# Optimization experiments

Hardware: AMD Instinct MI355X
Metric: run time of the kernel (lower is better)

The kernel has to match this reference:

```python
import jax, jax.numpy as jnp
import numpy as np

B, S, D = 2, 4096, 256
H, DH, DM = 8, 32, 1024
ROPE_BASE = 10000.0
LN_EPS = 1e-5


def _layer_norm(x, g, b):
    mu = jnp.mean(x, axis=-1, keepdims=True)
    var = jnp.mean(jnp.square(x - mu), axis=-1, keepdims=True)
    return (x - mu) * jax.lax.rsqrt(var + LN_EPS) * g + b


def _rope(x):
    # x: [b, s, h, d_head]; lucidrains interleaved-pair RoPE
    s, d = x.shape[1], x.shape[-1]
    inv_freq = 1.0 / (ROPE_BASE ** (jnp.arange(0, d, 2, dtype=jnp.float32) / d))  # [d/2]
    freqs = jnp.arange(s, dtype=jnp.float32)[:, None] * inv_freq[None, :]          # [s, d/2]
    freqs = jnp.repeat(freqs, 2, axis=-1)                                          # [s, d]
    cos = jnp.cos(freqs)[None, :, None, :]
    sin = jnp.sin(freqs)[None, :, None, :]
    x1, x2 = x[..., 0::2], x[..., 1::2]
    rot = jnp.stack((-x2, x1), axis=-1).reshape(x.shape)
    return x * cos + rot * sin


def setup_inputs() -> dict:
    key = jax.random.key(0)
    ks = jax.random.split(key, 8)
    sw = 1.0 / np.sqrt(D)
    return {
        "x": jax.random.normal(ks[0], (B, S, D), jnp.float32),
        "Wq": jax.random.normal(ks[1], (D, D), jnp.float32) * sw,
        "Wk": jax.random.normal(ks[2], (D, D), jnp.float32) * sw,
        "Wv": jax.random.normal(ks[3], (D, D), jnp.float32) * sw,
        "Wo": jax.random.normal(ks[4], (D, D), jnp.float32) * sw,
        "ln1_g": jnp.ones((D,), jnp.float32),
        "ln1_b": jnp.zeros((D,), jnp.float32),
        "ln2_g": jnp.ones((D,), jnp.float32),
        "ln2_b": jnp.zeros((D,), jnp.float32),
        "W2": jax.random.normal(ks[5], (DM, D), jnp.float32) * sw,
        "b2": jnp.zeros((DM,), jnp.float32),
        "W3": jax.random.normal(ks[6], (D, DM), jnp.float32) * (1.0 / np.sqrt(DM)),
        "b3": jnp.zeros((D,), jnp.float32),
    }


def reference(x, Wq, Wk, Wv, Wo, ln1_g, ln1_b, ln2_g, ln2_b, W2, b2, W3, b3):
    b, s, d = x.shape
    h, dh = H, DH
    xn = _layer_norm(x, ln1_g, ln1_b)
    q = (xn @ Wq.T).reshape(b, s, h, dh)
    k = (xn @ Wk.T).reshape(b, s, h, dh)
    v = (xn @ Wv.T).reshape(b, s, h, dh)
    q = _rope(q)
    k = _rope(k)
    # scores: [b, h, q, k] (full matrix, matching original implementation)
    scores = jnp.einsum('bqhd,bkhd->bhqk', q, k) / np.sqrt(dh)
    attn = jax.nn.softmax(scores, axis=-1)
    out = jnp.einsum('bhqk,bkhd->bqhd', attn, v).reshape(b, s, d)
    out = out @ Wo.T
    mlp_in = out + x
    y = _layer_norm(mlp_in, ln2_g, ln2_b)
    y = jax.nn.gelu(y @ W2.T + b2, approximate=False)
    y = y @ W3.T + b3
    return y + mlp_in
```

## Files before the change

kernel.cpp:

```cpp
#include <hip/hip_runtime.h>
#include <math.h>

#define D 256
#define S 4096
#define H 8
#define DH 32
#define DM 1024
#define NTOK 8192

typedef __attribute__((ext_vector_type(8))) short short8;
typedef __attribute__((ext_vector_type(4))) float f32x4;

#define QSCALE (0.17677669529663687f * 1.4426950408889634f)

__device__ inline unsigned short f2bf(float f) {
    union { float f; unsigned u; } v; v.f = f;
    unsigned r = v.u + 0x7fffu + ((v.u >> 16) & 1u);
    return (unsigned short)(r >> 16);
}
__device__ inline void gload16(const void* g, void* l) {
    __builtin_amdgcn_global_load_lds((const __attribute__((address_space(1))) void*)g,
                                     (__attribute__((address_space(3))) void*)l, 16, 0, 0);
}

__global__ void conv_all(const float* __restrict__ Wq, const float* __restrict__ Wk,
                         const float* __restrict__ Wv, const float* __restrict__ Wo,
                         const float* __restrict__ W2, const float* __restrict__ W3,
                         unsigned short* __restrict__ wqkv, unsigned short* __restrict__ wo_b,
                         unsigned short* __restrict__ w2_b, unsigned short* __restrict__ w3_b,
                         float* __restrict__ ct, float* __restrict__ st) {
    int i = blockIdx.x * 256 + threadIdx.x;
    if (i < 196608) {
        const float* s = (i < 65536) ? Wq : ((i < 131072) ? Wk : Wv);
        wqkv[i] = f2bf(s[i & 65535]);
    } else if (i < 262144) {
        wo_b[i - 196608] = f2bf(Wo[i - 196608]);
    } else if (i < 524288) {
        w2_b[i - 262144] = f2bf(W2[i - 262144]);
    } else if (i < 786432) {
        w3_b[i - 524288] = f2bf(W3[i - 524288]);
    } else {
        int j = i - 786432;
        int spos = j >> 4, pi = j & 15;
        float inv_freq = powf(10000.0f, -(float)(2 * pi) / 32.0f);
        float fr = (float)spos * inv_freq;
        ct[j] = cosf(fr);
        st[j] = sinf(fr);
    }
}

__global__ void ln_kernel(const float* __restrict__ x, const float* __restrict__ g,
                          const float* __restrict__ b, unsigned short* __restrict__ out) {
    __shared__ float red[8];
    int row = blockIdx.x;
    int tid = threadIdx.x;
    float v = x[(size_t)row * D + tid];
    float s = v, s2 = v * v;
    #pragma unroll
    for (int off = 32; off > 0; off >>= 1) {
        s  += __shfl_xor(s, off, 64);
        s2 += __shfl_xor(s2, off, 64);
    }
    int wave = tid >> 6;
    if ((tid & 63) == 0) { red[wave] = s; red[wave + 4] = s2; }
    __syncthreads();
    float sum   = red[0] + red[1] + red[2] + red[3];
    float sumsq = red[4] + red[5] + red[6] + red[7];
    float mu  = sum * (1.0f / D);
    float var = sumsq * (1.0f / D) - mu * mu;
    float rs  = rsqrtf(var + 1e-5f);
    out[(size_t)row * D + tid] = f2bf((v - mu) * rs * g[tid] + b[tid]);
}

__global__ __launch_bounds__(256) void gemm128(const unsigned short* __restrict__ A,
        const unsigned short* __restrict__ Bw, void* __restrict__ outp,
        unsigned short* __restrict__ vt,
        const float* __restrict__ bias, const float* __restrict__ res,
        const float* __restrict__ ct, const float* __restrict__ st,
        int N, int K, int mode) {
    __shared__ unsigned short As[2][128 * 32];
    __shared__ unsigned short Bs[2][64 * 32];
    int tid = threadIdx.x;
    int w = tid >> 6, l = tid & 63;
    int lm = l & 15, lg = l >> 4;
    int wm = (w >> 1) * 64, wn = (w & 1) * 32;
    int bm = blockIdx.x * 128, bn = blockIdx.y * 64;
    const unsigned short* Ag = A + (size_t)(bm + w * 16 + (l >> 2)) * K + ((l & 3) ^ ((l >> 3) & 3)) * 8;
    const unsigned short* Bg = Bw + (size_t)(bn + w * 16 + (l >> 2)) * K + ((l & 3) ^ ((l >> 3) & 3)) * 8;
    const int kswz = (lm >> 1) & 3;
    f32x4 acc[4][2] = {};

    gload16(Ag, &As[0][w * 512]);
    gload16(Ag + (size_t)64 * K, &As[0][2048 + w * 512]);
    gload16(Bg, &Bs[0][w * 512]);
    #pragma unroll 2
    for (int k0 = 0; k0 < K; k0 += 32) {
        int cur = (k0 >> 5) & 1;
        __syncthreads();
        if (k0 + 32 < K) {
            gload16(Ag + k0 + 32, &As[1 - cur][w * 512]);
            gload16(Ag + (size_t)64 * K + k0 + 32, &As[1 - cur][2048 + w * 512]);
            gload16(Bg + k0 + 32, &Bs[1 - cur][w * 512]);
        }
        short8 af[4], bf[2];
        #pragma unroll
        for (int i = 0; i < 4; ++i) af[i] = *(const short8*)&As[cur][(wm + i * 16 + lm) * 32 + (lg ^ kswz) * 8];
        #pragma unroll
        for (int i = 0; i < 2; ++i) bf[i] = *(const short8*)&Bs[cur][(wn + i * 16 + lm) * 32 + (lg ^ kswz) * 8];
        #pragma unroll
        for (int mi = 0; mi < 4; ++mi)
            #pragma unroll
            for (int ni = 0; ni < 2; ++ni)
                acc[mi][ni] = __builtin_amdgcn_mfma_f32_16x16x32_bf16(af[mi], bf[ni], acc[mi][ni], 0, 0, 0);
    }

    if (mode == 0) {
        if (bn >= 512) {
            #pragma unroll
            for (int mi = 0; mi < 4; ++mi) {
                #pragma unroll
                for (int ni = 0; ni < 2; ++ni) {
                    int ng = bn + wn + ni * 16 + lm - 512;
                    int hh = ng >> 5, dh = ng & 31;
                    int mg0 = bm + wm + mi * 16 + lg * 4;
                    int bb = mg0 >> 12, ss = mg0 & 4095;
                    ushort4 pv;
                    pv.x = f2bf(acc[mi][ni][0]); pv.y = f2bf(acc[mi][ni][1]);
                    pv.z = f2bf(acc[mi][ni][2]); pv.w = f2bf(acc[mi][ni][3]);
                    *(ushort4*)(vt + ((size_t)((bb * 8 + hh) * 32 + dh)) * S + ss) = pv;
                }
            }
        } else {
            #pragma unroll
            for (int mi = 0; mi < 4; ++mi) {
                #pragma unroll
                for (int ni = 0; ni < 2; ++ni) {
                    int ng = bn + wn + ni * 16 + lm;
                    int pi = (ng & 31) >> 1;
                    float sgn = (ng & 1) ? 1.f : -1.f;
                    float qs  = (ng < 256) ? QSCALE : 1.f;
                    #pragma unroll
                    for (int r2 = 0; r2 < 4; ++r2) {
                        int mg = bm + wm + mi * 16 + lg * 4 + r2;
                        int spos = mg & (S - 1);
                        float vv = acc[mi][ni][r2];
                        float pv = __shfl_xor(vv, 1, 64);
                        float cs = ct[spos * 16 + pi];
                        float sn = st[spos * 16 + pi];
                        float ov = (vv * cs + sgn * pv * sn) * qs;
                        ((unsigned short*)outp)[(size_t)mg * N + ng] = f2bf(ov);
                    }
                }
            }
        }
        return;
    }
    #pragma unroll
    for (int mi = 0; mi < 4; ++mi) {
        #pragma unroll
        for (int ni = 0; ni < 2; ++ni) {
            int ng = bn + wn + ni * 16 + lm;
            #pragma unroll
            for (int r2 = 0; r2 < 4; ++r2) {
                int mg = bm + wm + mi * 16 + lg * 4 + r2;
                float v = acc[mi][ni][r2];
                size_t idx = (size_t)mg * N + ng;
                if (mode == 1) {
                    ((float*)outp)[idx] = v + res[idx];
                } else if (mode == 2) {
                    float t = v + bias[ng];
                    ((unsigned short*)outp)[idx] = f2bf(0.5f * t * (1.0f + erff(t * 0.70710678118654752f)));
                } else {
                    ((float*)outp)[idx] = v + bias[ng] + res[idx];
                }
            }
        }
    }
}

__global__ __launch_bounds__(512) void attn_kernel(const unsigned short* __restrict__ Cq,
        const unsigned short* __restrict__ vt, unsigned short* __restrict__ out) {
    __shared__ unsigned short Ks[2][64][32];
    __shared__ unsigned short Vs[2][32][64];
    __shared__ unsigned short Ones[16][64];
    int tid = threadIdx.x;
    int w = tid >> 6, l = tid & 63;
    int lm = l & 15, lg = l >> 4;
    int qt = blockIdx.x & 31;
    int bh = blockIdx.x >> 5;
    int b = bh >> 3, h = bh & 7;
    int q0 = qt * 128 + w * 16;

    if (tid < 256) {
        unsigned short val = (tid < 16) ? (unsigned short)0x3F80 : (unsigned short)0;
        *(ushort4*)(&Ones[0][0] + tid * 4) = make_ushort4(val, val, val, val);
    }

    const short8 qf = *(const short8*)(Cq + ((size_t)(b * S + q0 + lm)) * 768 + h * DH + lg * 8);
    int ws = w & 3;
    int p = ws * 16 + (l >> 2);
    int krow = ((p >> 5) << 5) + (((p >> 2) & 3) << 3) + (((p >> 4) & 1) << 2) + (p & 3);
    const unsigned short* kg = Cq + ((size_t)(b * S)) * 768 + 256 + h * 32
                               + (size_t)krow * 768 + ((l & 3) ^ ((l >> 3) & 3)) * 8;
    const unsigned short* vg = vt + ((size_t)(bh * 32 + ws * 8 + (l >> 3))) * S + ((l & 7) ^ (l >> 3)) * 8;
    unsigned short* klds0 = &Ks[0][ws * 16][0];
    unsigned short* vlds0 = &Vs[0][ws * 8][0];
    unsigned short* klds1 = &Ks[1][ws * 16][0];
    unsigned short* vlds1 = &Vs[1][ws * 8][0];
    const int kswz = (lm >> 1) & 3;
    const int vswz = lm & 7;

    f32x4 o0 = {0.f, 0.f, 0.f, 0.f}, o1 = {0.f, 0.f, 0.f, 0.f}, o2 = {0.f, 0.f, 0.f, 0.f};
    const f32x4 z = {0.f, 0.f, 0.f, 0.f};

    if (w < 4) gload16(kg, klds0);
    else       gload16(vg, vlds0);

    #pragma unroll 2
    for (int it = 0; it < S / 64; ++it) {
        int cur = it & 1;
        __syncthreads();
        if (it + 1 < S / 64) {
            if (w < 4) gload16(kg + (size_t)(it + 1) * 64 * 768, cur ? klds0 : klds1);
            else       gload16(vg + (size_t)(it + 1) * 64,       cur ? vlds0 : vlds1);
        }
        #pragma unroll
        for (int half = 0; half < 2; ++half) {
            short8 kf0 = *(const short8*)&Ks[cur][half * 32 + lm][(lg ^ kswz) * 8];
            short8 kf1 = *(const short8*)&Ks[cur][half * 32 + 16 + lm][(lg ^ kswz) * 8];
            f32x4 s0 = __builtin_amdgcn_mfma_f32_16x16x32_bf16(kf0, qf, z, 0, 0, 0);
            f32x4 s1 = __builtin_amdgcn_mfma_f32_16x16x32_bf16(kf1, qf, z, 0, 0, 0);
            unsigned u0[4], u1[4];
            #pragma unroll
            for (int i = 0; i < 4; ++i) {
                union { float f; unsigned u; } c0, c1;
                c0.f = __builtin_amdgcn_exp2f(s0[i]);
                c1.f = __builtin_amdgcn_exp2f(s1[i]);
                u0[i] = c0.u;
                u1[i] = c1.u;
            }
            union { unsigned u[4]; short8 s; } pk;
            pk.u[0] = __builtin_amdgcn_perm(u0[1], u0[0], 0x07060302u);
            pk.u[1] = __builtin_amdgcn_perm(u0[3], u0[2], 0x07060302u);
            pk.u[2] = __builtin_amdgcn_perm(u1[1], u1[0], 0x07060302u);
            pk.u[3] = __builtin_amdgcn_perm(u1[3], u1[2], 0x07060302u);
            short8 pf = pk.s;
            int vc = ((half * 4 + lg) ^ vswz) * 8;
            short8 va0 = *(const short8*)&Vs[cur][lm][vc];
            short8 va1 = *(const short8*)&Vs[cur][16 + lm][vc];
            short8 va2 = *(const short8*)&Ones[lm][vc];
            o0 = __builtin_amdgcn_mfma_f32_16x16x32_bf16(va0, pf, o0, 0, 0, 0);
            o1 = __builtin_amdgcn_mfma_f32_16x16x32_bf16(va1, pf, o1, 0, 0, 0);
            o2 = __builtin_amdgcn_mfma_f32_16x16x32_bf16(va2, pf, o2, 0, 0, 0);
        }
    }
    float lsum = __shfl(o2[0], lm, 64);
    float inv = 1.0f / lsum;
    ushort4 r0, r1;
    r0.x = f2bf(o0[0] * inv); r0.y = f2bf(o0[1] * inv);
    r0.z = f2bf(o0[2] * inv); r0.w = f2bf(o0[3] * inv);
    r1.x = f2bf(o1[0] * inv); r1.y = f2bf(o1[1] * inv);
    r1.z = f2bf(o1[2] * inv); r1.w = f2bf(o1[3] * inv);
    unsigned short* ob = out + ((size_t)(b * S + q0 + lm)) * D + h * DH;
    *(ushort4*)(ob + lg * 4)      = r0;
    *(ushort4*)(ob + 16 + lg * 4) = r1;
}

extern "C" void kernel_launch(void* const* d_in, const int* in_sizes, int n_in,
                              void* d_out, int out_size, void* d_ws, size_t ws_size,
                              hipStream_t stream) {
    const float* x     = (const float*)d_in[0];
    const float* Wq    = (const float*)d_in[1];
    const float* Wk    = (const float*)d_in[2];
    const float* Wv    = (const float*)d_in[3];
    const float* Wo    = (const float*)d_in[4];
    const float* ln1_g = (const float*)d_in[5];
    const float* ln1_b = (const float*)d_in[6];
    const float* ln2_g = (const float*)d_in[7];
    const float* ln2_b = (const float*)d_in[8];
    const float* W2    = (const float*)d_in[9];
    const float* b2    = (const float*)d_in[10];
    const float* W3    = (const float*)d_in[11];
    const float* b3    = (const float*)d_in[12];

    char* w8 = (char*)d_ws;
    unsigned short* wqkv = (unsigned short*)(w8);
    unsigned short* wo_b = (unsigned short*)(w8 + 393216);
    unsigned short* w2_b = (unsigned short*)(w8 + 524288);
    unsigned short* w3_b = (unsigned short*)(w8 + 1048576);
    float*          ct   = (float*)(w8 + 1572864);
    float*          st   = (float*)(w8 + 1835008);
    unsigned short* xn   = (unsigned short*)(w8 + 2097152);
    unsigned short* Cq   = (unsigned short*)(w8 + 6291456);
    unsigned short* hb   = Cq;
    unsigned short* vtb  = (unsigned short*)(w8 + 23068672);
    unsigned short* ab   = (unsigned short*)(w8 + 27262976);
    float*          mlpin= (float*)(w8 + 31457280);
    unsigned short* yn   = xn;

    conv_all<<<3328, 256, 0, stream>>>(Wq, Wk, Wv, Wo, W2, W3, wqkv, wo_b, w2_b, w3_b, ct, st);
    ln_kernel<<<NTOK, 256, 0, stream>>>(x, ln1_g, ln1_b, xn);
    gemm128<<<dim3(64, 12), 256, 0, stream>>>(xn, wqkv, Cq, vtb, nullptr, nullptr, ct, st, 768, 256, 0);
    attn_kernel<<<512, 512, 0, stream>>>(Cq, vtb, ab);
    gemm128<<<dim3(64, 4), 256, 0, stream>>>(ab, wo_b, mlpin, nullptr, nullptr, x, nullptr, nullptr, 256, 256, 1);
    ln_kernel<<<NTOK, 256, 0, stream>>>(mlpin, ln2_g, ln2_b, yn);
    gemm128<<<dim3(64, 16), 256, 0, stream>>>(yn, w2_b, hb, nullptr, b2, nullptr, nullptr, nullptr, 1024, 256, 2);
    gemm128<<<dim3(64, 4), 256, 0, stream>>>(hb, w3_b, (float*)d_out, nullptr, b3, mlpin, nullptr, nullptr, 256, 1024, 3);
}
```

Measured before the change: 209.6 us.

## Replace double-buffered K-loop GEMM with 64x64 tiles loading full K=256 panels

The GEMM kernel changes from 128x64 tiles with a double-buffered 32-wide K pipeline to 64x64 tiles. Each tile loads a full 256-wide K panel of A and B into LDS (64 KB total) with an XOR swizzle, syncs once, then runs 8 MFMA k-steps. This removes the per-32-K barrier and doubles the grid to 128 row blocks for better CU fill. In exchange it loses load/compute overlap inside a block and uses more LDS per block, which can limit occupancy.

```diff
diff --git a/kernel.cpp b/kernel.cpp
--- a/kernel.cpp
+++ b/kernel.cpp
@@ -72,52 +72,56 @@
     out[(size_t)row * D + tid] = f2bf((v - mu) * rs * g[tid] + b[tid]);
 }
 
-__global__ __launch_bounds__(256) void gemm128(const unsigned short* __restrict__ A,
+__global__ __launch_bounds__(256) void gemm_fat(const unsigned short* __restrict__ A,
         const unsigned short* __restrict__ Bw, void* __restrict__ outp,
         unsigned short* __restrict__ vt,
         const float* __restrict__ bias, const float* __restrict__ res,
         const float* __restrict__ ct, const float* __restrict__ st,
         int N, int K, int mode) {
-    __shared__ unsigned short As[2][128 * 32];
-    __shared__ unsigned short Bs[2][64 * 32];
+    __shared__ unsigned short As[64 * 256];
+    __shared__ unsigned short Bs[64 * 256];
     int tid = threadIdx.x;
     int w = tid >> 6, l = tid & 63;
     int lm = l & 15, lg = l >> 4;
-    int wm = (w >> 1) * 64, wn = (w & 1) * 32;
-    int bm = blockIdx.x * 128, bn = blockIdx.y * 64;
-    const unsigned short* Ag = A + (size_t)(bm + w * 16 + (l >> 2)) * K + ((l & 3) ^ ((l >> 3) & 3)) * 8;
-    const unsigned short* Bg = Bw + (size_t)(bn + w * 16 + (l >> 2)) * K + ((l & 3) ^ ((l >> 3) & 3)) * 8;
-    const int kswz = (lm >> 1) & 3;
-    f32x4 acc[4][2] = {};
-
-    gload16(Ag, &As[0][w * 512]);
-    gload16(Ag + (size_t)64 * K, &As[0][2048 + w * 512]);
-    gload16(Bg, &Bs[0][w * 512]);
-    #pragma unroll 2
-    for (int k0 = 0; k0 < K; k0 += 32) {
-        int cur = (k0 >> 5) & 1;
+    int wm = (w >> 1) * 32, wn = (w & 1) * 32;
+    int bm = blockIdx.x * 64, bn = blockIdx.y * 64;
+    int row0 = tid >> 5, pc = tid & 31;
+    int pcx = (pc ^ (row0 & 7)) * 8;
+    const int swz = lm & 7;
+    f32x4 acc[2][2] = {};
+
+    for (int kp = 0; kp < K; kp += 256) {
+        if (kp) __syncthreads();
+        const unsigned short* Ag = A + (size_t)(bm + row0) * K + kp + pcx;
+        const unsigned short* Bg = Bw + (size_t)(bn + row0) * K + kp + pcx;
+        unsigned short* al = &As[w * 512];
+        unsigned short* bl = &Bs[w * 512];
+        #pragma unroll
+        for (int it = 0; it < 8; ++it) {
+            gload16(Ag + (size_t)it * 8 * K, al + it * 2048);
+            gload16(Bg + (size_t)it * 8 * K, bl + it * 2048);
+        }
         __syncthreads();
-        if (k0 + 32 < K) {
-            gload16(Ag + k0 + 32, &As[1 - cur][w * 512]);
-            gload16(Ag + (size_t)64 * K + k0 + 32, &As[1 - cur][2048 + w * 512]);
-            gload16(Bg + k0 + 32, &Bs[1 - cur][w * 512]);
-        }
-        short8 af[4], bf[2];
         #pragma unroll
-        for (int i = 0; i < 4; ++i) af[i] = *(const short8*)&As[cur][(wm + i * 16 + lm) * 32 + (lg ^ kswz) * 8];
-        #pragma unroll
-        for (int i = 0; i < 2; ++i) bf[i] = *(const short8*)&Bs[cur][(wn + i * 16 + lm) * 32 + (lg ^ kswz) * 8];
-        #pragma unroll
-        for (int mi = 0; mi < 4; ++mi)
-            #pragma unroll
-            for (int ni = 0; ni < 2; ++ni)
-                acc[mi][ni] = __builtin_amdgcn_mfma_f32_16x16x32_bf16(af[mi], bf[ni], acc[mi][ni], 0, 0, 0);
+        for (int kk = 0; kk < 8; ++kk) {
+            short8 af[2], bf[2];
+            int ch = ((kk * 4 + lg) ^ swz) * 8;
+            #pragma unroll
+            for (int i = 0; i < 2; ++i) af[i] = *(const short8*)&As[(wm + i * 16 + lm) * 256 + ch];
+            #pragma unroll
+            for (int i = 0; i < 2; ++i) bf[i] = *(const short8*)&Bs[(wn + i * 16 + lm) * 256 + ch];
+            #pragma unroll
+            for (int mi = 0; mi < 2; ++mi)
+                #pragma unroll
+                for (int ni = 0; ni < 2; ++ni)
+                    acc[mi][ni] = __builtin_amdgcn_mfma_f32_16x16x32_bf16(af[mi], bf[ni], acc[mi][ni], 0, 0, 0);
+        }
     }
 
     if (mode == 0) {
         if (bn >= 512) {
             #pragma unroll
-            for (int mi = 0; mi < 4; ++mi) {
+            for (int mi = 0; mi < 2; ++mi) {
                 #pragma unroll
                 for (int ni = 0; ni < 2; ++ni) {
                     int ng = bn + wn + ni * 16 + lm - 512;
@@ -132,7 +136,7 @@
             }
         } else {
             #pragma unroll
-            for (int mi = 0; mi < 4; ++mi) {
+            for (int mi = 0; mi < 2; ++mi) {
                 #pragma unroll
                 for (int ni = 0; ni < 2; ++ni) {
                     int ng = bn + wn + ni * 16 + lm;
@@ -156,7 +160,7 @@
         return;
     }
     #pragma unroll
-    for (int mi = 0; mi < 4; ++mi) {
+    for (int mi = 0; mi < 2; ++mi) {
         #pragma unroll
         for (int ni = 0; ni < 2; ++ni) {
             int ng = bn + wn + ni * 16 + lm;
@@ -300,10 +304,10 @@
 
     conv_all<<<3328, 256, 0, stream>>>(Wq, Wk, Wv, Wo, W2, W3, wqkv, wo_b, w2_b, w3_b, ct, st);
     ln_kernel<<<NTOK, 256, 0, stream>>>(x, ln1_g, ln1_b, xn);
-    gemm128<<<dim3(64, 12), 256, 0, stream>>>(xn, wqkv, Cq, vtb, nullptr, nullptr, ct, st, 768, 256, 0);
+    gemm_fat<<<dim3(128, 12), 256, 0, stream>>>(xn, wqkv, Cq, vtb, nullptr, nullptr, ct, st, 768, 256, 0);
     attn_kernel<<<512, 512, 0, stream>>>(Cq, vtb, ab);
-    gemm128<<<dim3(64, 4), 256, 0, stream>>>(ab, wo_b, mlpin, nullptr, nullptr, x, nullptr, nullptr, 256, 256, 1);
+    gemm_fat<<<dim3(128, 4), 256, 0, stream>>>(ab, wo_b, mlpin, nullptr, nullptr, x, nullptr, nullptr, 256, 256, 1);
     ln_kernel<<<NTOK, 256, 0, stream>>>(mlpin, ln2_g, ln2_b, yn);
-    gemm128<<<dim3(64, 16), 256, 0, stream>>>(yn, w2_b, hb, nullptr, b2, nullptr, nullptr, nullptr, 1024, 256, 2);
-    gemm128<<<dim3(64, 4), 256, 0, stream>>>(hb, w3_b, (float*)d_out, nullptr, b3, mlpin, nullptr, nullptr, 256, 1024, 3);
-}
+    gemm_fat<<<dim3(128, 16), 256, 0, stream>>>(yn, w2_b, hb, nullptr, b2, nullptr, nullptr, nullptr, 1024, 256, 2);
+    gemm_fat<<<dim3(128, 4), 256, 0, stream>>>(hb, w3_b, (float*)d_out, nullptr, b3, mlpin, nullptr, nullptr, 256, 1024, 3);
+}
```

After: 206.2 us. About the same (-1.6%).
